# Optimization experiments

Measured on AMD Instinct MI355X. Metric: run time of the kernel, lower is better.

Reference implementation:

```python
import jax, jax.numpy as jnp
import numpy as np

HID = 256  # hardcoded LSTM hidden size in the module


def _lstm_cell(x, h, c, W_ih, W_hh, b_ih, b_hh):
    # PyTorch gate order: i, f, g, o. x,h: [1,HID]; W_*: [4H,HID]; b_*: [4H]
    gates = x @ W_ih.T + h @ W_hh.T + b_ih + b_hh  # [1,4H]
    i, f, g, o = jnp.split(gates, 4, axis=-1)
    c_new = jax.nn.sigmoid(f) * c + jax.nn.sigmoid(i) * jnp.tanh(g)
    h_new = jax.nn.sigmoid(o) * jnp.tanh(c_new)
    return h_new, c_new


def setup_inputs() -> dict:
    key = jax.random.key(0)
    ks = jax.random.split(key, 9)
    s = 0.05
    return {
        "zm_1": jax.random.normal(ks[0], (1, HID), jnp.float32) * s,
        "W_ih": jax.random.normal(ks[1], (4 * HID, HID), jnp.float32) * s,
        "W_hh": jax.random.normal(ks[2], (4 * HID, HID), jnp.float32) * s,
        "b_ih": jax.random.normal(ks[3], (4 * HID,), jnp.float32) * s,
        "b_hh": jax.random.normal(ks[4], (4 * HID,), jnp.float32) * s,
        "W_loc": jax.random.normal(ks[5], (64, HID), jnp.float32) * s,
        "b_loc": jax.random.normal(ks[6], (64,), jnp.float32) * s,
        "W_scale": jax.random.normal(ks[7], (64, HID), jnp.float32) * s,
        "b_scale": jax.random.normal(ks[8], (64,), jnp.float32) * s,
        "K": 7,
        "batch_size": 32768,
    }


def reference(zm_1, W_ih, W_hh, b_ih, b_hh, W_loc, b_loc, W_scale, b_scale, K, batch_size):
    zm_size = W_loc.shape[0]
    h0 = jnp.zeros((1, HID), zm_1.dtype)
    c0 = jnp.zeros((1, HID), zm_1.dtype)

    def step(carry, _):
        x, h, c = carry
        h_new, c_new = _lstm_cell(x, h, c, W_ih, W_hh, b_ih, b_hh)
        # LSTM output z == h_new; it is also the next step's input
        return (h_new, h_new, c_new), h_new

    _, zs = jax.lax.scan(step, (zm_1, h0, c0), None, length=K - 1)  # [K-1,1,HID]
    p_z = jnp.concatenate([zm_1[None], zs], axis=0).reshape(K, HID)  # [K,HID]

    loc = p_z @ W_loc.T + b_loc        # [K,zm]
    scale = p_z @ W_scale.T + b_scale  # [K,zm]
    # repeat over batch dim -> [K*batch_size, zm]
    loc = jnp.broadcast_to(loc[:, None, :], (K, batch_size, zm_size)).reshape(-1, zm_size)
    scale = jnp.broadcast_to(scale[:, None, :], (K, batch_size, zm_size)).reshape(-1, zm_size)
    return loc, scale
```

## Files before the change

### kernel.cpp

```cpp
#include <hip/hip_runtime.h>
#include <cstdint>
#include <cstddef>

#define HID    256
#define NROW   1024
#define KSTEPS 7
#define ZM     64
#define BATCH  32768

typedef float f32x4 __attribute__((ext_vector_type(4)));

#define WS_GATES 0
#define WS_C     (6 * NROW)
#define WS_PZ    (6 * NROW + 7 * HID)
#define WS_TAB   (6 * NROW + 14 * HID)
#define WS_WSUM  (6 * NROW + 14 * HID + 896)

__device__ __forceinline__ float sigf(float x)       { return 1.0f / (1.0f + __expf(-x)); }
__device__ __forceinline__ float tanhf_fast(float x) { return 1.0f - 2.0f / (__expf(2.0f * x) + 1.0f); }

__device__ __forceinline__ float dot4(f32x4 a, f32x4 b) {
    return a.x * b.x + a.y * b.y + a.z * b.z + a.w * b.w;
}

__global__ __launch_bounds__(256) void init_kernel(
    const float* __restrict__ zm1,
    const float* __restrict__ Wih, const float* __restrict__ Whh,
    const float* __restrict__ bih, const float* __restrict__ bhh,
    float* __restrict__ ws)
{
    const int t = threadIdx.x, b = blockIdx.x;
    f32x4*       wsum4 = (f32x4*)(ws + WS_WSUM);
    const f32x4* a4    = (const f32x4*)Wih;
    const f32x4* c4    = (const f32x4*)Whh;
    const int id = b * 256 + t;
    wsum4[id] = a4[id] + c4[id];

    if (b == 0) {
        ws[WS_PZ + t] = zm1[t];
        ws[WS_C + t]  = 0.0f;
    }
    if (b < 64) {
        const int row = b * 16 + (t >> 4);
        const int l16 = t & 15;
        const f32x4* w4 = (const f32x4*)(Wih + (size_t)row * HID);
        const f32x4* x4 = (const f32x4*)zm1;
        float part = 0.f;
        #pragma unroll
        for (int kk = 0; kk < 4; ++kk) part += dot4(w4[l16 * 4 + kk], x4[l16 * 4 + kk]);
        part += __shfl_xor(part, 1);
        part += __shfl_xor(part, 2);
        part += __shfl_xor(part, 4);
        part += __shfl_xor(part, 8);
        if (l16 == 0) ws[WS_GATES + row] = part + bih[row] + bhh[row];
    }
}

__global__ __launch_bounds__(256) void step_kernel(
    const float* __restrict__ bih, const float* __restrict__ bhh,
    float* __restrict__ ws, int s)
{
    __shared__ float hsh[HID];
    const int t = threadIdx.x, b = blockIdx.x;
    {
        const float* gp = ws + WS_GATES + (size_t)(s - 1) * NROW;
        float gi = gp[t], gf = gp[HID + t], gg = gp[2 * HID + t], go = gp[3 * HID + t];
        float cp = ws[WS_C + (size_t)(s - 1) * HID + t];
        float cn = sigf(gf) * cp + sigf(gi) * tanhf_fast(gg);
        float h  = sigf(go) * tanhf_fast(cn);
        ws[WS_C + (size_t)s * HID + t] = cn;
        if (b == 0) ws[WS_PZ + (size_t)s * HID + t] = h;
        hsh[t] = h;
    }
    __syncthreads();
    const int row = b * 16 + (t >> 4);
    const int l16 = t & 15;
    const f32x4* w4 = (const f32x4*)(ws + WS_WSUM + (size_t)row * HID);
    const f32x4* h4 = (const f32x4*)hsh;
    float part = 0.f;
    #pragma unroll
    for (int kk = 0; kk < 4; ++kk) part += dot4(w4[l16 * 4 + kk], h4[l16 * 4 + kk]);
    part += __shfl_xor(part, 1);
    part += __shfl_xor(part, 2);
    part += __shfl_xor(part, 4);
    part += __shfl_xor(part, 8);
    if (l16 == 0) ws[WS_GATES + (size_t)s * NROW + row] = part + bih[row] + bhh[row];
}

__global__ __launch_bounds__(256) void final_kernel(
    const float* __restrict__ Wloc, const float* __restrict__ bloc,
    const float* __restrict__ Wsc,  const float* __restrict__ bsc,
    float* __restrict__ ws)
{
    __shared__ float hsh[HID];
    const int t = threadIdx.x, b = blockIdx.x;
    {
        const float* gp = ws + WS_GATES + (size_t)5 * NROW;
        float gi = gp[t], gf = gp[HID + t], gg = gp[2 * HID + t], go = gp[3 * HID + t];
        float cp = ws[WS_C + (size_t)5 * HID + t];
        float cn = sigf(gf) * cp + sigf(gi) * tanhf_fast(gg);
        hsh[t] = sigf(go) * tanhf_fast(cn);
    }
    __syncthreads();
    const int wm    = b;
    const int which = wm / KSTEPS;
    const int m     = wm % KSTEPS;
    const int j     = t >> 2;
    const int q     = t & 3;
    const float* W  = which ? Wsc : Wloc;
    const float  bb = which ? bsc[j] : bloc[j];
    const f32x4* w4 = (const f32x4*)(W + (size_t)j * HID);
    const f32x4* p4 = (m == 6) ? (const f32x4*)hsh
                               : (const f32x4*)(ws + WS_PZ + (size_t)m * HID);
    float acc = 0.f;
    #pragma unroll
    for (int kk = 0; kk < 16; ++kk) acc += dot4(w4[q * 16 + kk], p4[q * 16 + kk]);
    acc += __shfl_xor(acc, 1);
    acc += __shfl_xor(acc, 2);
    if (q == 0) ws[WS_TAB + wm * ZM + j] = acc + bb;
}

__global__ __launch_bounds__(256) void bcast_kernel(
    const float* __restrict__ tab, f32x4* __restrict__ out)
{
    const int bid   = blockIdx.x;
    const int wm    = bid >> 7;
    const int chunk = bid & 127;
    const f32x4* t4 = (const f32x4*)tab;
    const f32x4 v = t4[wm * 16 + (threadIdx.x & 15)];
    size_t base = (size_t)wm * (BATCH * ZM / 4) + (size_t)chunk * 4096 + threadIdx.x;
    #pragma unroll
    for (int k = 0; k < 16; ++k) {
        __builtin_nontemporal_store(v, &out[base + (size_t)k * 256]);
    }
}

extern "C" void kernel_launch(void* const* d_in, const int* in_sizes, int n_in,
                              void* d_out, int out_size, void* d_ws, size_t ws_size,
                              hipStream_t stream) {
    const float* zm1  = (const float*)d_in[0];
    const float* Wih  = (const float*)d_in[1];
    const float* Whh  = (const float*)d_in[2];
    const float* bih  = (const float*)d_in[3];
    const float* bhh  = (const float*)d_in[4];
    const float* Wloc = (const float*)d_in[5];
    const float* bloc = (const float*)d_in[6];
    const float* Wsc  = (const float*)d_in[7];
    const float* bsc  = (const float*)d_in[8];
    float* ws = (float*)d_ws;

    init_kernel<<<256, 256, 0, stream>>>(zm1, Wih, Whh, bih, bhh, ws);
    for (int s = 1; s <= 5; ++s)
        step_kernel<<<64, 256, 0, stream>>>(bih, bhh, ws, s);
    final_kernel<<<14, 256, 0, stream>>>(Wloc, bloc, Wsc, bsc, ws);
    bcast_kernel<<<14 * 128, 256, 0, stream>>>(ws + WS_TAB, (f32x4*)d_out);
}
```

Baseline: 166.2 us.

## Fuse LSTM recurrence into one cooperative kernel with grid sync and register weights

Replaces the init, per-step and final kernels with a single cooperative kernel that uses grid.sync between LSTM steps. Each thread keeps its slice of W_ih+W_hh and its cell state in registers, so the summed-weight workspace and the c-state array are no longer written or read. This removes several kernel launches and their gaps. In exchange it adds grid-wide barrier cost and requires cooperative launch residency.

Measured after the change: 258.5 us. 1.56x slower.

```diff
diff --git a/kernel.cpp b/kernel.cpp
--- a/kernel.cpp
+++ b/kernel.cpp
@@ -1,6 +1,9 @@
 #include <hip/hip_runtime.h>
+#include <hip/hip_cooperative_groups.h>
 #include <cstdint>
 #include <cstddef>
+
+namespace cg = cooperative_groups;
 
 #define HID    256
 #define NROW   1024
@@ -11,10 +14,8 @@
 typedef float f32x4 __attribute__((ext_vector_type(4)));
 
 #define WS_GATES 0
-#define WS_C     (6 * NROW)
-#define WS_PZ    (6 * NROW + 7 * HID)
-#define WS_TAB   (6 * NROW + 14 * HID)
-#define WS_WSUM  (6 * NROW + 14 * HID + 896)
+#define WS_PZ    (6 * NROW)
+#define WS_TAB   (6 * NROW + 7 * HID)
 
 __device__ __forceinline__ float sigf(float x)       { return 1.0f / (1.0f + __expf(-x)); }
 __device__ __forceinline__ float tanhf_fast(float x) { return 1.0f - 2.0f / (__expf(2.0f * x) + 1.0f); }
@@ -23,101 +24,91 @@
     return a.x * b.x + a.y * b.y + a.z * b.z + a.w * b.w;
 }
 
-__global__ __launch_bounds__(256) void init_kernel(
+__global__ __launch_bounds__(256) void chain_kernel(
     const float* __restrict__ zm1,
     const float* __restrict__ Wih, const float* __restrict__ Whh,
     const float* __restrict__ bih, const float* __restrict__ bhh,
+    const float* __restrict__ Wloc, const float* __restrict__ bloc,
+    const float* __restrict__ Wsc,  const float* __restrict__ bsc,
     float* __restrict__ ws)
 {
-    const int t = threadIdx.x, b = blockIdx.x;
-    f32x4*       wsum4 = (f32x4*)(ws + WS_WSUM);
-    const f32x4* a4    = (const f32x4*)Wih;
-    const f32x4* c4    = (const f32x4*)Whh;
-    const int id = b * 256 + t;
-    wsum4[id] = a4[id] + c4[id];
+    cg::grid_group grid = cg::this_grid();
+    const int t   = threadIdx.x, b = blockIdx.x;
+    const int row = b * 16 + (t >> 4);
+    const int l16 = t & 15;
+    __shared__ float hsh[HID];
 
-    if (b == 0) {
-        ws[WS_PZ + t] = zm1[t];
-        ws[WS_C + t]  = 0.0f;
-    }
-    if (b < 64) {
-        const int row = b * 16 + (t >> 4);
-        const int l16 = t & 15;
-        const f32x4* w4 = (const f32x4*)(Wih + (size_t)row * HID);
-        const f32x4* x4 = (const f32x4*)zm1;
+    const f32x4* wi4 = (const f32x4*)(Wih + (size_t)row * HID + l16 * 16);
+    const f32x4* wh4 = (const f32x4*)(Whh + (size_t)row * HID + l16 * 16);
+    f32x4 wsum[4];
+    #pragma unroll
+    for (int kk = 0; kk < 4; ++kk) wsum[kk] = wi4[kk] + wh4[kk];
+    const float bihr = bih[row], bhhr = bhh[row];
+
+    {
+        const f32x4* x4 = (const f32x4*)(zm1 + l16 * 16);
         float part = 0.f;
         #pragma unroll
-        for (int kk = 0; kk < 4; ++kk) part += dot4(w4[l16 * 4 + kk], x4[l16 * 4 + kk]);
+        for (int kk = 0; kk < 4; ++kk) part += dot4(wi4[kk], x4[kk]);
         part += __shfl_xor(part, 1);
         part += __shfl_xor(part, 2);
         part += __shfl_xor(part, 4);
         part += __shfl_xor(part, 8);
-        if (l16 == 0) ws[WS_GATES + row] = part + bih[row] + bhh[row];
+        if (l16 == 0) ws[WS_GATES + row] = part + bihr + bhhr;
     }
-}
+    if (b == 0) ws[WS_PZ + t] = zm1[t];
 
-__global__ __launch_bounds__(256) void step_kernel(
-    const float* __restrict__ bih, const float* __restrict__ bhh,
-    float* __restrict__ ws, int s)
-{
-    __shared__ float hsh[HID];
-    const int t = threadIdx.x, b = blockIdx.x;
-    {
+    float c_reg = 0.0f;
+    __threadfence();
+    grid.sync();
+
+    #pragma unroll 1
+    for (int s = 1; s <= 5; ++s) {
         const float* gp = ws + WS_GATES + (size_t)(s - 1) * NROW;
         float gi = gp[t], gf = gp[HID + t], gg = gp[2 * HID + t], go = gp[3 * HID + t];
-        float cp = ws[WS_C + (size_t)(s - 1) * HID + t];
-        float cn = sigf(gf) * cp + sigf(gi) * tanhf_fast(gg);
-        float h  = sigf(go) * tanhf_fast(cn);
-        ws[WS_C + (size_t)s * HID + t] = cn;
+        float cn = sigf(gf) * c_reg + sigf(gi) * tanhf_fast(gg);
+        c_reg = cn;
+        float h = sigf(go) * tanhf_fast(cn);
         if (b == 0) ws[WS_PZ + (size_t)s * HID + t] = h;
         hsh[t] = h;
+        __syncthreads();
+
+        float p = 0.f;
+        const f32x4* h4 = (const f32x4*)hsh + l16 * 4;
+        #pragma unroll
+        for (int kk = 0; kk < 4; ++kk) p += dot4(wsum[kk], h4[kk]);
+        p += __shfl_xor(p, 1);
+        p += __shfl_xor(p, 2);
+        p += __shfl_xor(p, 4);
+        p += __shfl_xor(p, 8);
+        if (l16 == 0) ws[WS_GATES + (size_t)s * NROW + row] = p + bihr + bhhr;
+        __threadfence();
+        grid.sync();
     }
-    __syncthreads();
-    const int row = b * 16 + (t >> 4);
-    const int l16 = t & 15;
-    const f32x4* w4 = (const f32x4*)(ws + WS_WSUM + (size_t)row * HID);
-    const f32x4* h4 = (const f32x4*)hsh;
-    float part = 0.f;
-    #pragma unroll
-    for (int kk = 0; kk < 4; ++kk) part += dot4(w4[l16 * 4 + kk], h4[l16 * 4 + kk]);
-    part += __shfl_xor(part, 1);
-    part += __shfl_xor(part, 2);
-    part += __shfl_xor(part, 4);
-    part += __shfl_xor(part, 8);
-    if (l16 == 0) ws[WS_GATES + (size_t)s * NROW + row] = part + bih[row] + bhh[row];
-}
 
-__global__ __launch_bounds__(256) void final_kernel(
-    const float* __restrict__ Wloc, const float* __restrict__ bloc,
-    const float* __restrict__ Wsc,  const float* __restrict__ bsc,
-    float* __restrict__ ws)
-{
-    __shared__ float hsh[HID];
-    const int t = threadIdx.x, b = blockIdx.x;
-    {
+    if (b < 14) {
         const float* gp = ws + WS_GATES + (size_t)5 * NROW;
         float gi = gp[t], gf = gp[HID + t], gg = gp[2 * HID + t], go = gp[3 * HID + t];
-        float cp = ws[WS_C + (size_t)5 * HID + t];
-        float cn = sigf(gf) * cp + sigf(gi) * tanhf_fast(gg);
+        float cn = sigf(gf) * c_reg + sigf(gi) * tanhf_fast(gg);
         hsh[t] = sigf(go) * tanhf_fast(cn);
+        __syncthreads();
+        const int wm    = b;
+        const int which = wm / KSTEPS;
+        const int m     = wm % KSTEPS;
+        const int j     = t >> 2;
+        const int q     = t & 3;
+        const float* W  = which ? Wsc : Wloc;
+        const float  bb = which ? bsc[j] : bloc[j];
+        const f32x4* w4 = (const f32x4*)(W + (size_t)j * HID);
+        const f32x4* p4 = (m == 6) ? (const f32x4*)hsh
+                                   : (const f32x4*)(ws + WS_PZ + (size_t)m * HID);
+        float acc = 0.f;
+        #pragma unroll
+        for (int kk = 0; kk < 16; ++kk) acc += dot4(w4[q * 16 + kk], p4[q * 16 + kk]);
+        acc += __shfl_xor(acc, 1);
+        acc += __shfl_xor(acc, 2);
+        if (q == 0) ws[WS_TAB + wm * ZM + j] = acc + bb;
     }
-    __syncthreads();
-    const int wm    = b;
-    const int which = wm / KSTEPS;
-    const int m     = wm % KSTEPS;
-    const int j     = t >> 2;
-    const int q     = t & 3;
-    const float* W  = which ? Wsc : Wloc;
-    const float  bb = which ? bsc[j] : bloc[j];
-    const f32x4* w4 = (const f32x4*)(W + (size_t)j * HID);
-    const f32x4* p4 = (m == 6) ? (const f32x4*)hsh
-                               : (const f32x4*)(ws + WS_PZ + (size_t)m * HID);
-    float acc = 0.f;
-    #pragma unroll
-    for (int kk = 0; kk < 16; ++kk) acc += dot4(w4[q * 16 + kk], p4[q * 16 + kk]);
-    acc += __shfl_xor(acc, 1);
-    acc += __shfl_xor(acc, 2);
-    if (q == 0) ws[WS_TAB + wm * ZM + j] = acc + bb;
 }
 
 __global__ __launch_bounds__(256) void bcast_kernel(
@@ -149,9 +140,9 @@
     const float* bsc  = (const float*)d_in[8];
     float* ws = (float*)d_ws;
 
-    init_kernel<<<256, 256, 0, stream>>>(zm1, Wih, Whh, bih, bhh, ws);
-    for (int s = 1; s <= 5; ++s)
-        step_kernel<<<64, 256, 0, stream>>>(bih, bhh, ws, s);
-    final_kernel<<<14, 256, 0, stream>>>(Wloc, bloc, Wsc, bsc, ws);
+    void* args[] = { (void*)&zm1, (void*)&Wih, (void*)&Whh, (void*)&bih, (void*)&bhh,
+                     (void*)&Wloc, (void*)&bloc, (void*)&Wsc, (void*)&bsc, (void*)&ws };
+    hipLaunchCooperativeKernel((const void*)chain_kernel, dim3(64), dim3(256),
+                               args, 0, stream);
     bcast_kernel<<<14 * 128, 256, 0, stream>>>(ws + WS_TAB, (f32x4*)d_out);
 }
```
